# Kernel optimization log

Measured on AMD Instinct MI355X. Metric: run time of the kernel, lower is better.

## Reference

```python
import jax, jax.numpy as jnp
import numpy as np
from jax import lax

DIM = 64
NUM_HEAD = 8  # head_dim in the torch code
NUM_HEADS = DIM // NUM_HEAD          # 8 heads
HEAD_DIM = (DIM // 2) // NUM_HEADS   # 4 = NUM_HEAD // 2
SCALE = NUM_HEAD ** (-0.5)
GROUPS = DIM // 2


def _conv3x3x3(x, w):
    # grouped Conv3d: in=DIM, out=DIM//2, groups=DIM//2 (2 in-ch per group), pad 1
    return lax.conv_general_dilated(
        x, w, window_strides=(1, 1, 1), padding=[(1, 1)] * 3,
        dimension_numbers=('NCDHW', 'OIDHW', 'NCDHW'),
        feature_group_count=GROUPS)


def _conv1x1x1(x, w):
    # grouped Conv3d: in=DIM//2, out=DIM, groups=DIM//2 (1 in-ch, 2 out-ch per group)
    return lax.conv_general_dilated(
        x, w, window_strides=(1, 1, 1), padding=[(0, 0)] * 3,
        dimension_numbers=('NCDHW', 'OIDHW', 'NCDHW'),
        feature_group_count=GROUPS)


def setup_inputs() -> dict:
    key = jax.random.key(0)
    ks = jax.random.split(key, 6)
    b, B, h, w = 8, 5, 128, 128
    x = jax.random.normal(ks[0], (b, DIM, B, h, w), dtype=jnp.float32)
    last = jax.random.normal(ks[1], (b, DIM, B, h, w), dtype=jnp.float32)
    wq = jax.random.normal(ks[2], (DIM // 2, 2, 3, 3, 3), dtype=jnp.float32) * 0.05
    wk = jax.random.normal(ks[3], (DIM // 2, 2, 3, 3, 3), dtype=jnp.float32) * 0.05
    wv = jax.random.normal(ks[4], (DIM // 2, 2, 3, 3, 3), dtype=jnp.float32) * 0.05
    wproj = jax.random.normal(ks[5], (DIM, 1, 1, 1, 1), dtype=jnp.float32) * 0.3
    return {"x": x, "last": last, "wq": wq, "wk": wk, "wv": wv, "wproj": wproj}


def reference(x, last, wq, wk, wv, wproj):
    q = _conv3x3x3(x, wq)      # (b, C, B, h, w), C = DIM//2
    k = _conv3x3x3(last, wk)
    v = _conv3x3x3(last, wv)
    b, C, B, h, w = q.shape
    n = b * h * w

    def to_heads(t):
        # 'b c B h w -> (b h w) B c' then split c into (heads, d) and put heads first
        t = jnp.transpose(t, (0, 3, 4, 2, 1)).reshape(n, B, NUM_HEADS, HEAD_DIM)
        return jnp.transpose(t, (0, 2, 1, 3))  # (n, heads, B, d)

    qh, kh, vh = to_heads(q), to_heads(k), to_heads(v)
    attn = jax.nn.softmax(jnp.einsum('nhid,nhjd->nhij', qh * SCALE, kh), axis=-1)
    out = jnp.einsum('nhij,nhjd->nhid', attn, vh)          # (n, heads, B, d)
    out = jnp.transpose(out, (0, 2, 1, 3)).reshape(b, h, w, B, C)
    out = jnp.transpose(out, (0, 4, 3, 1, 2))              # (b, C, B, h, w)
    return _conv1x1x1(out, wproj)                          # (b, DIM, B, h, w)
```

## Files before the change

### kernel.cpp

```cpp
#include <hip/hip_runtime.h>


#define WD   128
#define HWs  (128 * 128)
#define BD   5
#define CS   (BD * HWs)

__global__ __launch_bounds__(256, 2)
void TCA_49177375539279_kernel(const float* __restrict__ x,
                               const float* __restrict__ last,
                               const float* __restrict__ wq,
                               const float* __restrict__ wk,
                               const float* __restrict__ wv,
                               const float* __restrict__ wp,
                               float* __restrict__ out)
{
    const int z  = blockIdx.z;
    const int bi = z >> 3;
    const int hd = z & 7;
    const int px = (blockIdx.x << 6) + (threadIdx.x & 63);
    const int py = (blockIdx.y << 2) + (threadIdx.x >> 6);

    const int ch0     = hd << 3;
    const int base_in = (bi * 64 + ch0) * CS;

    const float* __restrict__ wqb = wq + hd * 216;
    const float* __restrict__ wkb = wk + hd * 216;
    const float* __restrict__ wvb = wv + hd * 216;

    float q[4][BD], k[4][BD], v[4][BD];
#pragma unroll
    for (int c = 0; c < 4; ++c)
#pragma unroll
        for (int i = 0; i < BD; ++i) { q[c][i] = 0.f; k[c][i] = 0.f; v[c][i] = 0.f; }

#pragma unroll 1
    for (int dy = 0; dy < 3; ++dy) {
        const int yy = py + dy - 1;
#pragma unroll
        for (int dx = 0; dx < 3; ++dx) {
            const int xx = px + dx - 1;
            const bool ok = ((unsigned)yy < 128u) && ((unsigned)xx < 128u);
            const int sp = yy * WD + xx;
            float xi[8][BD];
#pragma unroll
            for (int ic = 0; ic < 8; ++ic)
#pragma unroll
                for (int d = 0; d < BD; ++d)
                    xi[ic][d] = ok ? x[base_in + ic * CS + d * HWs + sp] : 0.f;
#pragma unroll
            for (int c = 0; c < 4; ++c)
#pragma unroll
                for (int j = 0; j < 2; ++j) {
                    const float* wr = wqb + (c * 2 + j) * 27 + dy * 3 + dx;
#pragma unroll
                    for (int dz = 0; dz < 3; ++dz) {
                        const float wgt = wr[dz * 9];
#pragma unroll
                        for (int i = 0; i < BD; ++i) {
                            const int d = i + dz - 1;
                            if (d >= 0 && d < BD)
                                q[c][i] = fmaf(wgt, xi[c * 2 + j][d], q[c][i]);
                        }
                    }
                }
        }
    }

#pragma unroll 1
    for (int dy = 0; dy < 3; ++dy) {
        const int yy = py + dy - 1;
#pragma unroll
        for (int dx = 0; dx < 3; ++dx) {
            const int xx = px + dx - 1;
            const bool ok = ((unsigned)yy < 128u) && ((unsigned)xx < 128u);
            const int sp = yy * WD + xx;
            float li[8][BD];
#pragma unroll
            for (int ic = 0; ic < 8; ++ic)
#pragma unroll
                for (int d = 0; d < BD; ++d)
                    li[ic][d] = ok ? last[base_in + ic * CS + d * HWs + sp] : 0.f;
#pragma unroll
            for (int c = 0; c < 4; ++c)
#pragma unroll
                for (int j = 0; j < 2; ++j) {
                    const float* wrk = wkb + (c * 2 + j) * 27 + dy * 3 + dx;
                    const float* wrv = wvb + (c * 2 + j) * 27 + dy * 3 + dx;
#pragma unroll
                    for (int dz = 0; dz < 3; ++dz) {
                        const float wk_ = wrk[dz * 9];
                        const float wv_ = wrv[dz * 9];
#pragma unroll
                        for (int i = 0; i < BD; ++i) {
                            const int d = i + dz - 1;
                            if (d >= 0 && d < BD) {
                                k[c][i] = fmaf(wk_, li[c * 2 + j][d], k[c][i]);
                                v[c][i] = fmaf(wv_, li[c * 2 + j][d], v[c][i]);
                            }
                        }
                    }
                }
        }
    }

    const float SCALE = 0.35355339059327373f;
    float p[BD][BD];
#pragma unroll
    for (int i = 0; i < BD; ++i) {
        float s[BD];
        float m = -3.0e38f;
#pragma unroll
        for (int j = 0; j < BD; ++j) {
            float t = q[0][i] * k[0][j];
            t = fmaf(q[1][i], k[1][j], t);
            t = fmaf(q[2][i], k[2][j], t);
            t = fmaf(q[3][i], k[3][j], t);
            t *= SCALE;
            s[j] = t;
            m = fmaxf(m, t);
        }
        float sum = 0.f;
#pragma unroll
        for (int j = 0; j < BD; ++j) { float e = __expf(s[j] - m); p[i][j] = e; sum += e; }
        const float r = 1.0f / sum;
#pragma unroll
        for (int j = 0; j < BD; ++j) p[i][j] *= r;
    }

    const int sp0   = py * WD + px;
    const int obase = base_in + sp0;
#pragma unroll
    for (int c = 0; c < 4; ++c) {
        const float w0 = wp[ch0 + 2 * c];
        const float w1 = wp[ch0 + 2 * c + 1];
#pragma unroll
        for (int i = 0; i < BD; ++i) {
            float o = p[i][0] * v[c][0];
            o = fmaf(p[i][1], v[c][1], o);
            o = fmaf(p[i][2], v[c][2], o);
            o = fmaf(p[i][3], v[c][3], o);
            o = fmaf(p[i][4], v[c][4], o);
            out[obase + (2 * c)     * CS + i * HWs] = w0 * o;
            out[obase + (2 * c + 1) * CS + i * HWs] = w1 * o;
        }
    }
}

extern "C" void kernel_launch(void* const* d_in, const int* in_sizes, int n_in,
                              void* d_out, int out_size, void* d_ws, size_t ws_size,
                              hipStream_t stream)
{
    const float* x    = (const float*)d_in[0];
    const float* last = (const float*)d_in[1];
    const float* wq   = (const float*)d_in[2];
    const float* wk   = (const float*)d_in[3];
    const float* wv   = (const float*)d_in[4];
    const float* wp   = (const float*)d_in[5];
    float* out = (float*)d_out;

    dim3 grid(2, 32, 64);
    dim3 block(256);
    hipLaunchKernelGGL(TCA_49177375539279_kernel, grid, block, 0, stream,
                       x, last, wq, wk, wv, wp, out);
}
```

Before: 567.1 us.

## Use raw buffer loads with hardware OOB zero-fill and remap blocks to single-row wavefronts

Replaces the predicated global loads with AMD raw buffer loads. Per-row buffer descriptors set their record count to zero for out-of-range rows, and a huge offset handles the left edge, so the hardware returns zeros for padding without branching. The loop order becomes per input channel and depth slice, loading a 3x3 neighbourhood once and reusing it across the three dz taps. Blocks shrink to 64 threads with a 1D grid swizzled to interleave heads and batches across the device, and stores go through buffer stores with scalar offsets. The main risks are relying on buffer OOB semantics and the config word being correct for this hardware, plus extra launch granularity.

```diff
diff --git a/kernel.cpp b/kernel.cpp
--- a/kernel.cpp
+++ b/kernel.cpp
@@ -1,12 +1,55 @@
 #include <hip/hip_runtime.h>
 
 
-#define WD   128
-#define HWs  (128 * 128)
-#define BD   5
-#define CS   (BD * HWs)
+#define WD    128
+#define HWn   (128 * 128)
+#define BD    5
+#define CS    (BD * HWn)
+#define CFGW  0x00020000u
 
-__global__ __launch_bounds__(256, 2)
+typedef int v4i __attribute__((ext_vector_type(4)));
+
+__device__ float amd_buf_load_f32(v4i rsrc, int voffset, int soffset, int aux)
+    __asm("llvm.amdgcn.raw.buffer.load.f32");
+__device__ void amd_buf_store_f32(float data, v4i rsrc, int voffset, int soffset, int aux)
+    __asm("llvm.amdgcn.raw.buffer.store.f32");
+
+union SRD {
+    v4i v;
+    struct { const void* base; unsigned nr; unsigned cfg; } s;
+};
+static_assert(sizeof(SRD) == 16, "SRD must be 16 bytes");
+
+__device__ __forceinline__ void load9(const char* rb, unsigned nr_t, unsigned nr_b,
+                                      int vl, int vcn, int vr, float t[9])
+{
+    SRD r0, r1, r2;
+    r0.s.base = rb;        r0.s.nr = nr_t; r0.s.cfg = CFGW;
+    r1.s.base = rb + 512;  r1.s.nr = 512u; r1.s.cfg = CFGW;
+    r2.s.base = rb + 1024; r2.s.nr = nr_b; r2.s.cfg = CFGW;
+    t[0] = amd_buf_load_f32(r0.v, vl,  0, 0);
+    t[1] = amd_buf_load_f32(r0.v, vcn, 0, 0);
+    t[2] = amd_buf_load_f32(r0.v, vr,  0, 0);
+    t[3] = amd_buf_load_f32(r1.v, vl,  0, 0);
+    t[4] = amd_buf_load_f32(r1.v, vcn, 0, 0);
+    t[5] = amd_buf_load_f32(r1.v, vr,  0, 0);
+    t[6] = amd_buf_load_f32(r2.v, vl,  0, 0);
+    t[7] = amd_buf_load_f32(r2.v, vcn, 0, 0);
+    t[8] = amd_buf_load_f32(r2.v, vr,  0, 0);
+}
+
+#define FMA9(acc, W, T)                 \
+    acc = fmaf((W)[0], (T)[0], acc);    \
+    acc = fmaf((W)[1], (T)[1], acc);    \
+    acc = fmaf((W)[2], (T)[2], acc);    \
+    acc = fmaf((W)[3], (T)[3], acc);    \
+    acc = fmaf((W)[4], (T)[4], acc);    \
+    acc = fmaf((W)[5], (T)[5], acc);    \
+    acc = fmaf((W)[6], (T)[6], acc);    \
+    acc = fmaf((W)[7], (T)[7], acc);    \
+    acc = fmaf((W)[8], (T)[8], acc);
+
+__global__ __launch_bounds__(64, 4)
 void TCA_49177375539279_kernel(const float* __restrict__ x,
                                const float* __restrict__ last,
                                const float* __restrict__ wq,
@@ -15,92 +58,76 @@
                                const float* __restrict__ wp,
                                float* __restrict__ out)
 {
-    const int z  = blockIdx.z;
+    const int f  = (int)blockIdx.x;
+    const int w  = ((f & 7) << 11) | (f >> 3);
+    const int bx = w & 1;
+    const int py = (w >> 1) & 127;
+    const int z  = w >> 8;
     const int bi = z >> 3;
     const int hd = z & 7;
-    const int px = (blockIdx.x << 6) + (threadIdx.x & 63);
-    const int py = (blockIdx.y << 2) + (threadIdx.x >> 6);
+    const int px = (bx << 6) + (int)threadIdx.x;
 
-    const int ch0     = hd << 3;
-    const int base_in = (bi * 64 + ch0) * CS;
+    const int    ch0     = hd << 3;
+    const size_t base_in = (size_t)(bi * 64 + ch0) * CS;
+    const float* xb = x    + base_in;
+    const float* lb = last + base_in;
 
-    const float* __restrict__ wqb = wq + hd * 216;
-    const float* __restrict__ wkb = wk + hd * 216;
-    const float* __restrict__ wvb = wv + hd * 216;
+    const int vcn = px << 2;
+    const int vl  = (px == 0) ? (int)0x80000000 : (vcn - 4);
+    const int vr  = vcn + 4;
 
-    float q[4][BD], k[4][BD], v[4][BD];
+    const unsigned nr_t = (py >= 1)   ? 512u : 0u;
+    const unsigned nr_b = (py <= 126) ? 512u : 0u;
+    const int row_off   = (py - 1) * 512;
+
+    float q[4][BD] = {};
 #pragma unroll
-    for (int c = 0; c < 4; ++c)
+    for (int ic = 0; ic < 8; ++ic) {
+        const int c = ic >> 1;
+        const float* wqi = wq + hd * 216 + ic * 27;
 #pragma unroll
-        for (int i = 0; i < BD; ++i) { q[c][i] = 0.f; k[c][i] = 0.f; v[c][i] = 0.f; }
-
-#pragma unroll 1
-    for (int dy = 0; dy < 3; ++dy) {
-        const int yy = py + dy - 1;
+        for (int d = 0; d < BD; ++d) {
+            float t[9];
+            load9((const char*)(xb + (size_t)(ic * BD + d) * HWn) + row_off,
+                  nr_t, nr_b, vl, vcn, vr, t);
 #pragma unroll
-        for (int dx = 0; dx < 3; ++dx) {
-            const int xx = px + dx - 1;
-            const bool ok = ((unsigned)yy < 128u) && ((unsigned)xx < 128u);
-            const int sp = yy * WD + xx;
-            float xi[8][BD];
-#pragma unroll
-            for (int ic = 0; ic < 8; ++ic)
-#pragma unroll
-                for (int d = 0; d < BD; ++d)
-                    xi[ic][d] = ok ? x[base_in + ic * CS + d * HWs + sp] : 0.f;
-#pragma unroll
-            for (int c = 0; c < 4; ++c)
-#pragma unroll
-                for (int j = 0; j < 2; ++j) {
-                    const float* wr = wqb + (c * 2 + j) * 27 + dy * 3 + dx;
-#pragma unroll
-                    for (int dz = 0; dz < 3; ++dz) {
-                        const float wgt = wr[dz * 9];
-#pragma unroll
-                        for (int i = 0; i < BD; ++i) {
-                            const int d = i + dz - 1;
-                            if (d >= 0 && d < BD)
-                                q[c][i] = fmaf(wgt, xi[c * 2 + j][d], q[c][i]);
-                        }
-                    }
+            for (int dz = 0; dz < 3; ++dz) {
+                const int i = d + 1 - dz;
+                if (i >= 0 && i < BD) {
+                    const float* wz = wqi + dz * 9;
+                    float a = q[c][i];
+                    FMA9(a, wz, t);
+                    q[c][i] = a;
                 }
+            }
         }
     }
 
-#pragma unroll 1
-    for (int dy = 0; dy < 3; ++dy) {
-        const int yy = py + dy - 1;
+    float k[4][BD] = {}, v[4][BD] = {};
 #pragma unroll
-        for (int dx = 0; dx < 3; ++dx) {
-            const int xx = px + dx - 1;
-            const bool ok = ((unsigned)yy < 128u) && ((unsigned)xx < 128u);
-            const int sp = yy * WD + xx;
-            float li[8][BD];
+    for (int ic = 0; ic < 8; ++ic) {
+        const int c = ic >> 1;
+        const float* wki = wk + hd * 216 + ic * 27;
+        const float* wvi = wv + hd * 216 + ic * 27;
 #pragma unroll
-            for (int ic = 0; ic < 8; ++ic)
+        for (int d = 0; d < BD; ++d) {
+            float t[9];
+            load9((const char*)(lb + (size_t)(ic * BD + d) * HWn) + row_off,
+                  nr_t, nr_b, vl, vcn, vr, t);
 #pragma unroll
-                for (int d = 0; d < BD; ++d)
-                    li[ic][d] = ok ? last[base_in + ic * CS + d * HWs + sp] : 0.f;
-#pragma unroll
-            for (int c = 0; c < 4; ++c)
-#pragma unroll
-                for (int j = 0; j < 2; ++j) {
-                    const float* wrk = wkb + (c * 2 + j) * 27 + dy * 3 + dx;
-                    const float* wrv = wvb + (c * 2 + j) * 27 + dy * 3 + dx;
-#pragma unroll
-                    for (int dz = 0; dz < 3; ++dz) {
-                        const float wk_ = wrk[dz * 9];
-                        const float wv_ = wrv[dz * 9];
-#pragma unroll
-                        for (int i = 0; i < BD; ++i) {
-                            const int d = i + dz - 1;
-                            if (d >= 0 && d < BD) {
-                                k[c][i] = fmaf(wk_, li[c * 2 + j][d], k[c][i]);
-                                v[c][i] = fmaf(wv_, li[c * 2 + j][d], v[c][i]);
-                            }
-                        }
-                    }
+            for (int dz = 0; dz < 3; ++dz) {
+                const int i = d + 1 - dz;
+                if (i >= 0 && i < BD) {
+                    const float* wzk = wki + dz * 9;
+                    const float* wzv = wvi + dz * 9;
+                    float a = k[c][i];
+                    FMA9(a, wzk, t);
+                    k[c][i] = a;
+                    float b = v[c][i];
+                    FMA9(b, wzv, t);
+                    v[c][i] = b;
                 }
+            }
         }
     }
 
@@ -128,8 +155,11 @@
         for (int j = 0; j < BD; ++j) p[i][j] *= r;
     }
 
-    const int sp0   = py * WD + px;
-    const int obase = base_in + sp0;
+    SRD ro;
+    ro.s.base = out + base_in;
+    ro.s.nr   = (unsigned)(41943040u - (unsigned)base_in) * 4u;
+    ro.s.cfg  = CFGW;
+    const int sob = (py * WD) << 2;
 #pragma unroll
     for (int c = 0; c < 4; ++c) {
         const float w0 = wp[ch0 + 2 * c];
@@ -141,8 +171,10 @@
             o = fmaf(p[i][2], v[c][2], o);
             o = fmaf(p[i][3], v[c][3], o);
             o = fmaf(p[i][4], v[c][4], o);
-            out[obase + (2 * c)     * CS + i * HWs] = w0 * o;
-            out[obase + (2 * c + 1) * CS + i * HWs] = w1 * o;
+            amd_buf_store_f32(w0 * o, ro.v, vcn,
+                              sob + (((2 * c)     * CS + i * HWn) << 2), 0);
+            amd_buf_store_f32(w1 * o, ro.v, vcn,
+                              sob + (((2 * c + 1) * CS + i * HWn) << 2), 0);
         }
     }
 }
@@ -159,8 +191,8 @@
     const float* wp   = (const float*)d_in[5];
     float* out = (float*)d_out;
 
-    dim3 grid(2, 32, 64);
-    dim3 block(256);
+    dim3 grid(16384);
+    dim3 block(64);
     hipLaunchKernelGGL(TCA_49177375539279_kernel, grid, block, 0, stream,
                        x, last, wq, wk, wv, wp, out);
 }
```

Result: slower. 821.1 us (+44.8%).
